# Kernel tuning notes

Hardware: AMD Instinct MI355X
Metric: run time of the kernel (lower is better)

## Reference

```python
import jax, jax.numpy as jnp
import numpy as np

N_NODES = 100000
N_EDGES = 1600000
K = 4
D = 16  # d_in // K
NEG_SLOPE = 0.01  # F.leaky_relu default
EPS = 1e-12       # F.normalize default eps


def setup_inputs() -> dict:
    key = jax.random.key(0)
    k1, k2, k3 = jax.random.split(key, 3)
    f_in = jax.random.normal(k1, (N_NODES, K, D), dtype=jnp.float32)
    edges = jax.random.randint(k2, (N_EDGES, 2), 0, N_NODES, dtype=jnp.int64)
    attn_w = jax.random.normal(k3, (K, 2 * D), dtype=jnp.float32) * 0.1
    return {"f_in": f_in, "edges": edges, "attn_w": attn_w}


def reference(f_in, edges, attn_w):
    # f_in: [N, K, D], edges: [E, 2] (src, dst), attn_w: [K, 2D]
    src = edges[:, 0]
    dst = edges[:, 1]
    f_src = f_in[src]            # [E, K, D] gather
    f_dst = f_in[dst]            # [E, K, D] gather
    f_edge = jnp.concatenate([f_src, f_dst], axis=2)  # [E, K, 2D]
    # per-factor attention score + leaky_relu
    score = jnp.einsum('ekd,kd->ek', f_edge, attn_w)  # [E, K]
    score = jnp.where(score >= 0, score, NEG_SLOPE * score)
    # scatter_softmax over edges grouped by src, per factor
    smax = jax.ops.segment_max(score, src, num_segments=N_NODES)  # [N, K]
    smax = jnp.where(jnp.isfinite(smax), smax, 0.0)  # empty segments -> -inf -> 0
    ex = jnp.exp(score - smax[src])                               # [E, K]
    denom = jax.ops.segment_sum(ex, src, num_segments=N_NODES)    # [N, K]
    norm = ex / denom[src]                                        # [E, K]
    # weighted scatter_add of neighbor embeddings
    m = jax.ops.segment_sum(f_dst * norm[:, :, None], src, num_segments=N_NODES)  # [N, K, D]
    # F.normalize(m): L2 over dim=1 (factor axis)
    l2 = jnp.sqrt(jnp.sum(m * m, axis=1, keepdims=True))  # [N, 1, D]
    return m / jnp.maximum(l2, EPS)
```

## Files before the change

kernel.cpp:

```cpp
#include <hip/hip_runtime.h>

#define N_NODES 100000
#define N_EDGES 1600000
#define KH 4
#define DH 16
#define KD (KH * DH)
#define MAXDEG 64
#define NEG_SLOPE 0.01f

#define T 256
#define NPART 8
#define PART_SZ ((N_NODES + NPART - 1) / NPART)
#define SCORE_BLOCKS 1568
#define SCATTER_PB 256
#define SCATTER_BLOCKS (SCATTER_PB * NPART)
#define AGG_BLOCKS ((PART_SZ / 4) * NPART)

__device__ __forceinline__ float lrelu(float x) {
    return (x >= 0.f) ? x : NEG_SLOPE * x;
}

__global__ void k_pre(const float* __restrict__ f_in,
                      const float* __restrict__ attn_w,
                      const int* __restrict__ edges,
                      float* __restrict__ a_src,
                      float* __restrict__ a_dst,
                      int* __restrict__ deg,
                      int* __restrict__ dst_pad) {
    if (blockIdx.x < SCORE_BLOCKS) {
        int i = blockIdx.x * T + threadIdx.x;
        if (i >= N_NODES * KH) return;
        int k = i & (KH - 1);
        const float4* f  = (const float4*)(f_in + (size_t)i * DH);
        const float4* w1 = (const float4*)(attn_w + k * 2 * DH);
        const float4* w2 = (const float4*)(attn_w + k * 2 * DH + DH);
        float s1 = 0.f, s2 = 0.f;
#pragma unroll
        for (int j = 0; j < DH / 4; ++j) {
            float4 fv = f[j];
            float4 av = w1[j];
            float4 bv = w2[j];
            s1 += fv.x * av.x + fv.y * av.y + fv.z * av.z + fv.w * av.w;
            s2 += fv.x * bv.x + fv.y * bv.y + fv.z * bv.z + fv.w * bv.w;
        }
        a_src[i] = s1;
        a_dst[i] = s2;
    } else {
        int sb = blockIdx.x - SCORE_BLOCKS;
        int p  = sb & (NPART - 1);
        int q  = sb >> 3;
        int lo = p * PART_SZ;
        int hi = lo + PART_SZ;
        const long long* e2 = (const long long*)edges;
        const int npair = N_EDGES / 2;
        for (int i = q * T + threadIdx.x; i < npair; i += SCATTER_PB * T) {
            long long v0 = __builtin_nontemporal_load(&e2[2 * i]);
            long long v1 = __builtin_nontemporal_load(&e2[2 * i + 1]);
            int s0 = (int)(v0 & 0xffffffffLL);
            int d0 = (int)(v0 >> 32);
            int s1 = (int)(v1 & 0xffffffffLL);
            int d1 = (int)(v1 >> 32);
            if (s0 >= lo && s0 < hi) {
                int pos = atomicAdd(&deg[s0], 1);
                if (pos < MAXDEG)
                    dst_pad[(size_t)s0 * MAXDEG + pos] = d0;
            }
            if (s1 >= lo && s1 < hi) {
                int pos = atomicAdd(&deg[s1], 1);
                if (pos < MAXDEG)
                    dst_pad[(size_t)s1 * MAXDEG + pos] = d1;
            }
        }
    }
}

__global__ void k_node_aggregate(const int* __restrict__ deg,
                                 const int* __restrict__ dst_pad,
                                 const float* __restrict__ a_src,
                                 const float* __restrict__ a_dst,
                                 const float* __restrict__ f_in,
                                 float* __restrict__ out) {
    int p    = blockIdx.x & (NPART - 1);
    int q    = blockIdx.x >> 3;
    int wid  = threadIdx.x >> 6;
    int lane = threadIdx.x & 63;
    int n    = p * PART_SZ + q * 4 + wid;
    if (n >= N_NODES) return;
    int k = lane >> 4;

    int dg = deg[n];
    if (dg > MAXDEG) dg = MAXDEG;
    float as = a_src[n * KH + k];
    const int* dl = dst_pad + (size_t)n * MAXDEG;

    float acc = 0.f, dsum = 0.f;
    int i = 0;
    int dg8 = dg & ~7;
    for (; i < dg8; i += 8) {
        int4 da = *(const int4*)(dl + i);
        int4 db = *(const int4*)(dl + i + 4);
        float a0 = a_dst[da.x * KH + k];
        float a1 = a_dst[da.y * KH + k];
        float a2 = a_dst[da.z * KH + k];
        float a3 = a_dst[da.w * KH + k];
        float a4 = a_dst[db.x * KH + k];
        float a5 = a_dst[db.y * KH + k];
        float a6 = a_dst[db.z * KH + k];
        float a7 = a_dst[db.w * KH + k];
        float f0 = f_in[(size_t)da.x * KD + lane];
        float f1 = f_in[(size_t)da.y * KD + lane];
        float f2 = f_in[(size_t)da.z * KD + lane];
        float f3 = f_in[(size_t)da.w * KD + lane];
        float f4 = f_in[(size_t)db.x * KD + lane];
        float f5 = f_in[(size_t)db.y * KD + lane];
        float f6 = f_in[(size_t)db.z * KD + lane];
        float f7 = f_in[(size_t)db.w * KD + lane];
        float e0 = __expf(lrelu(as + a0));
        float e1 = __expf(lrelu(as + a1));
        float e2 = __expf(lrelu(as + a2));
        float e3 = __expf(lrelu(as + a3));
        float e4 = __expf(lrelu(as + a4));
        float e5 = __expf(lrelu(as + a5));
        float e6 = __expf(lrelu(as + a6));
        float e7 = __expf(lrelu(as + a7));
        dsum += ((e0 + e1) + (e2 + e3)) + ((e4 + e5) + (e6 + e7));
        acc  += e0 * f0 + e1 * f1 + e2 * f2 + e3 * f3
              + e4 * f4 + e5 * f5 + e6 * f6 + e7 * f7;
    }
    for (; i < dg; ++i) {
        int d = dl[i];
        float ex = __expf(lrelu(as + a_dst[d * KH + k]));
        dsum += ex;
        acc  += ex * f_in[(size_t)d * KD + lane];
    }

    float v = (dsum > 0.f) ? (acc / dsum) : 0.f;
    float ss = v * v;
    ss += __shfl_xor(ss, 16);
    ss += __shfl_xor(ss, 32);
    float inv = 1.f / fmaxf(sqrtf(ss), 1e-12f);
    out[(size_t)n * KD + lane] = v * inv;
}

extern "C" void kernel_launch(void* const* d_in, const int* in_sizes, int n_in,
                              void* d_out, int out_size, void* d_ws, size_t ws_size,
                              hipStream_t stream) {
    const float* f_in   = (const float*)d_in[0];
    const int*   edges  = (const int*)d_in[1];
    const float* attn_w = (const float*)d_in[2];
    float* out = (float*)d_out;

    float* a_src  = (float*)d_ws;
    float* a_dst  = a_src + N_NODES * KH;
    int*   deg    = (int*)(a_dst + N_NODES * KH);
    int*   dst_pad= deg + N_NODES;

    (void)hipMemsetAsync(deg, 0, (size_t)N_NODES * sizeof(int), stream);

    k_pre<<<SCORE_BLOCKS + SCATTER_BLOCKS, T, 0, stream>>>(f_in, attn_w, edges,
                                                           a_src, a_dst, deg, dst_pad);
    k_node_aggregate<<<AGG_BLOCKS, T, 0, stream>>>(deg, dst_pad, a_src, a_dst, f_in, out);
}
```

Before: 237.4 us.

## Split node aggregation wavefront into four edge groups with float4 row loads

Result: faster. 228.6 us (-3.7%).

```diff
diff --git a/kernel.cpp b/kernel.cpp
--- a/kernel.cpp
+++ b/kernel.cpp
@@ -86,60 +86,70 @@
     int lane = threadIdx.x & 63;
     int n    = p * PART_SZ + q * 4 + wid;
     if (n >= N_NODES) return;
-    int k = lane >> 4;
+    int g  = lane >> 4;
+    int m  = lane & 15;
+    int kk = m >> 2;
 
     int dg = deg[n];
     if (dg > MAXDEG) dg = MAXDEG;
-    float as = a_src[n * KH + k];
+    float as = a_src[n * KH + kk];
     const int* dl = dst_pad + (size_t)n * MAXDEG;
 
-    float acc = 0.f, dsum = 0.f;
+    float4 acc = make_float4(0.f, 0.f, 0.f, 0.f);
+    float dsum = 0.f;
     int i = 0;
     int dg8 = dg & ~7;
     for (; i < dg8; i += 8) {
-        int4 da = *(const int4*)(dl + i);
-        int4 db = *(const int4*)(dl + i + 4);
-        float a0 = a_dst[da.x * KH + k];
-        float a1 = a_dst[da.y * KH + k];
-        float a2 = a_dst[da.z * KH + k];
-        float a3 = a_dst[da.w * KH + k];
-        float a4 = a_dst[db.x * KH + k];
-        float a5 = a_dst[db.y * KH + k];
-        float a6 = a_dst[db.z * KH + k];
-        float a7 = a_dst[db.w * KH + k];
-        float f0 = f_in[(size_t)da.x * KD + lane];
-        float f1 = f_in[(size_t)da.y * KD + lane];
-        float f2 = f_in[(size_t)da.z * KD + lane];
-        float f3 = f_in[(size_t)da.w * KD + lane];
-        float f4 = f_in[(size_t)db.x * KD + lane];
-        float f5 = f_in[(size_t)db.y * KD + lane];
-        float f6 = f_in[(size_t)db.z * KD + lane];
-        float f7 = f_in[(size_t)db.w * KD + lane];
-        float e0 = __expf(lrelu(as + a0));
-        float e1 = __expf(lrelu(as + a1));
-        float e2 = __expf(lrelu(as + a2));
-        float e3 = __expf(lrelu(as + a3));
-        float e4 = __expf(lrelu(as + a4));
-        float e5 = __expf(lrelu(as + a5));
-        float e6 = __expf(lrelu(as + a6));
-        float e7 = __expf(lrelu(as + a7));
-        dsum += ((e0 + e1) + (e2 + e3)) + ((e4 + e5) + (e6 + e7));
-        acc  += e0 * f0 + e1 * f1 + e2 * f2 + e3 * f3
-              + e4 * f4 + e5 * f5 + e6 * f6 + e7 * f7;
+        int dA = dl[i + g];
+        int dB = dl[i + 4 + g];
+        float4 fA = *(const float4*)(f_in + (size_t)dA * KD + 4 * m);
+        float4 fB = *(const float4*)(f_in + (size_t)dB * KD + 4 * m);
+        float aA = a_dst[dA * KH + kk];
+        float aB = a_dst[dB * KH + kk];
+        float eA = __expf(lrelu(as + aA));
+        float eB = __expf(lrelu(as + aB));
+        dsum += eA + eB;
+        acc.x += eA * fA.x + eB * fB.x;
+        acc.y += eA * fA.y + eB * fB.y;
+        acc.z += eA * fA.z + eB * fB.z;
+        acc.w += eA * fA.w + eB * fB.w;
     }
-    for (; i < dg; ++i) {
-        int d = dl[i];
-        float ex = __expf(lrelu(as + a_dst[d * KH + k]));
-        dsum += ex;
-        acc  += ex * f_in[(size_t)d * KD + lane];
+    for (; i < dg; i += 4) {
+        if (i + g < dg) {
+            int d = dl[i + g];
+            float4 fv = *(const float4*)(f_in + (size_t)d * KD + 4 * m);
+            float e = __expf(lrelu(as + a_dst[d * KH + kk]));
+            dsum += e;
+            acc.x += e * fv.x;
+            acc.y += e * fv.y;
+            acc.z += e * fv.z;
+            acc.w += e * fv.w;
+        }
     }
 
-    float v = (dsum > 0.f) ? (acc / dsum) : 0.f;
-    float ss = v * v;
-    ss += __shfl_xor(ss, 16);
-    ss += __shfl_xor(ss, 32);
-    float inv = 1.f / fmaxf(sqrtf(ss), 1e-12f);
-    out[(size_t)n * KD + lane] = v * inv;
+    dsum  += __shfl_xor(dsum, 16);  dsum  += __shfl_xor(dsum, 32);
+    acc.x += __shfl_xor(acc.x, 16); acc.x += __shfl_xor(acc.x, 32);
+    acc.y += __shfl_xor(acc.y, 16); acc.y += __shfl_xor(acc.y, 32);
+    acc.z += __shfl_xor(acc.z, 16); acc.z += __shfl_xor(acc.z, 32);
+    acc.w += __shfl_xor(acc.w, 16); acc.w += __shfl_xor(acc.w, 32);
+
+    float invd = (dsum > 0.f) ? (1.f / dsum) : 0.f;
+    float4 v = make_float4(acc.x * invd, acc.y * invd, acc.z * invd, acc.w * invd);
+
+    float sx = v.x * v.x, sy = v.y * v.y, sz = v.z * v.z, sw = v.w * v.w;
+    sx += __shfl_xor(sx, 4); sx += __shfl_xor(sx, 8);
+    sy += __shfl_xor(sy, 4); sy += __shfl_xor(sy, 8);
+    sz += __shfl_xor(sz, 4); sz += __shfl_xor(sz, 8);
+    sw += __shfl_xor(sw, 4); sw += __shfl_xor(sw, 8);
+    float ix = 1.f / fmaxf(sqrtf(sx), 1e-12f);
+    float iy = 1.f / fmaxf(sqrtf(sy), 1e-12f);
+    float iz = 1.f / fmaxf(sqrtf(sz), 1e-12f);
+    float iw = 1.f / fmaxf(sqrtf(sw), 1e-12f);
+
+    if (g == 0) {
+        float4 o = make_float4(v.x * ix, v.y * iy, v.z * iz, v.w * iw);
+        *(float4*)(out + (size_t)n * KD + 4 * m) = o;
+    }
 }
 
 extern "C" void kernel_launch(void* const* d_in, const int* in_sizes, int n_in,
```
